# Kernel tuning notes

Hardware: AMD Instinct MI355X
Metric: run time of the kernel (lower is better)

## Reference

```python
import jax, jax.numpy as jnp
import numpy as np
from jax import lax

B, S = 64, 512
CHAR_N, CTYPE_N, BICHAR_N = 20000, 8, 200000
EXTCHAR_N, EXTBICHAR_N = 20000, 200000
D_CHAR, D_EXTCHAR, D_BICHAR, D_EXTBICHAR, D_CTYPE = 200, 200, 200, 200, 50
IN_DIM = D_CHAR + D_EXTCHAR + D_BICHAR + D_EXTBICHAR + D_CTYPE  # 850
HID, RNN_H = 512, 512


def setup_inputs() -> dict:
    key = jax.random.key(0)
    ks = jax.random.split(key, 24)
    idx = lambda k, n: jax.random.randint(k, (B, S), 0, n, dtype=jnp.int32)
    w = lambda k, shape: (jax.random.normal(k, shape, dtype=jnp.float32) * 0.02)
    return {
        'char_idx': idx(ks[0], CHAR_N),
        'char_type_idx': idx(ks[1], CTYPE_N),
        'leftbichar_idx': idx(ks[2], BICHAR_N),
        'rightbichar_idx': idx(ks[3], BICHAR_N),
        'extchar_idx': idx(ks[4], EXTCHAR_N),
        'leftextbichar_idx': idx(ks[5], EXTBICHAR_N),
        'rightextbichar_idx': idx(ks[6], EXTBICHAR_N),
        'charEmb': w(ks[7], (CHAR_N, D_CHAR)),
        'charTypeEmb': w(ks[8], (CTYPE_N, D_CTYPE)),
        'bicharEmb': w(ks[9], (BICHAR_N, D_BICHAR)),
        'extCharEmb': w(ks[10], (EXTCHAR_N, D_EXTCHAR)),
        'extBiCharEmb': w(ks[11], (EXTBICHAR_N, D_EXTBICHAR)),
        'W_lin': w(ks[12], (HID, IN_DIM)),
        'b_lin': w(ks[13], (HID,)),
        'W_ih_l': w(ks[14], (4 * RNN_H, HID)),
        'W_hh_l': w(ks[15], (4 * RNN_H, RNN_H)),
        'b_ih_l': w(ks[16], (4 * RNN_H,)),
        'b_hh_l': w(ks[17], (4 * RNN_H,)),
        'W_ih_r': w(ks[18], (4 * RNN_H, HID)),
        'W_hh_r': w(ks[19], (4 * RNN_H, RNN_H)),
        'b_ih_r': w(ks[20], (4 * RNN_H,)),
        'b_hh_r': w(ks[21], (4 * RNN_H,)),
    }


def _lstm(xg_sb4h, W_hh, reverse):
    # xg_sb4h: [S, B, 4H] precomputed input-to-gate projections (+ both biases)
    def step(carry, g_in):
        h, c = carry
        g = g_in + h @ W_hh.T  # [B, 4H]
        i, f, gg, o = jnp.split(g, 4, axis=-1)
        c = jax.nn.sigmoid(f) * c + jax.nn.sigmoid(i) * jnp.tanh(gg)
        h = jax.nn.sigmoid(o) * jnp.tanh(c)
        return (h, c), h
    h0 = jnp.zeros((xg_sb4h.shape[1], W_hh.shape[1]), xg_sb4h.dtype)
    _, hs = lax.scan(step, (h0, h0), xg_sb4h, reverse=reverse)
    return hs  # [S, B, H], hs[t] = hidden emitted at position t


def _encoder_fwd(char_idx, char_type_idx, leftbichar_idx, rightbichar_idx,
                 extchar_idx, leftextbichar_idx, rightextbichar_idx,
                 charEmb, charTypeEmb, bicharEmb, extCharEmb, extBiCharEmb,
                 W_lin, b_lin, W_ih_l, W_hh_l, b_ih_l, b_hh_l,
                 W_ih_r, W_hh_r, b_ih_r, b_hh_r):
    char = charEmb[char_idx]            # [B,S,200]
    ctype = charTypeEmb[char_type_idx]  # [B,S,50]
    extChar = extCharEmb[extchar_idx]
    leftBi = bicharEmb[leftbichar_idx]
    rightBi = bicharEmb[rightbichar_idx]
    leftExtBi = extBiCharEmb[leftextbichar_idx]
    rightExtBi = extBiCharEmb[rightextbichar_idx]
    # dropout is identity in eval mode
    leftCat = jnp.concatenate([char, extChar, leftBi, leftExtBi, ctype], axis=-1)
    rightCat = jnp.concatenate([char, extChar, rightBi, rightExtBi, ctype], axis=-1)
    leftIn = jnp.tanh(leftCat @ W_lin.T + b_lin)    # [B,S,HID]
    rightIn = jnp.tanh(rightCat @ W_lin.T + b_lin)  # [B,S,HID]
    xg_l = (jnp.einsum('bsh,gh->sbg', leftIn, W_ih_l) + b_ih_l + b_hh_l)
    xg_r = (jnp.einsum('bsh,gh->sbg', rightIn, W_ih_r) + b_ih_r + b_hh_r)
    hs_l = _lstm(xg_l, W_hh_l, reverse=False).swapaxes(0, 1)  # [B,S,RNN_H]
    hs_r = _lstm(xg_r, W_hh_r, reverse=True).swapaxes(0, 1)   # [B,S,RNN_H]
    return jnp.concatenate([hs_l, hs_r], axis=-1)  # [B,S,2*RNN_H]


def reference(char_idx, char_type_idx, leftbichar_idx, rightbichar_idx,
              extchar_idx, leftextbichar_idx, rightextbichar_idx,
              charEmb, charTypeEmb, bicharEmb, extCharEmb, extBiCharEmb,
              W_lin, b_lin, W_ih_l, W_hh_l, b_ih_l, b_hh_l,
              W_ih_r, W_hh_r, b_ih_r, b_hh_r):
    return _encoder_fwd(char_idx, char_type_idx, leftbichar_idx, rightbichar_idx,
                        extchar_idx, leftextbichar_idx, rightextbichar_idx,
                        charEmb, charTypeEmb, bicharEmb, extCharEmb, extBiCharEmb,
                        W_lin, b_lin, W_ih_l, W_hh_l, b_ih_l, b_hh_l,
                        W_ih_r, W_hh_r, b_ih_r, b_hh_r)
```

## Files before the change

### kernel.cpp

```cpp
#include <hip/hip_runtime.h>

#define INPUTS_BF16 0
#define OUT_BF16    0

typedef unsigned int  u32;
typedef unsigned short u16;
typedef unsigned long long u64;
typedef short bf16x8 __attribute__((ext_vector_type(8)));
typedef float f32x4  __attribute__((ext_vector_type(4)));
typedef unsigned int u32x4 __attribute__((ext_vector_type(4)));

__device__ __forceinline__ float bf2f(u16 x) {
  return __uint_as_float(((u32)x) << 16);
}
__device__ __forceinline__ u16 f2bf(float f) {
  u32 u = __float_as_uint(f);
  u += 0x7fffu + ((u >> 16) & 1u);
  return (u16)(u >> 16);
}

__device__ __forceinline__ u32 tload2(const void* tab, long idx2) {
#if INPUTS_BF16
  return ((const u32*)tab)[idx2];
#else
  float2 v = ((const float2*)tab)[idx2];
  return (u32)f2bf(v.x) | ((u32)f2bf(v.y) << 16);
#endif
}
__device__ __forceinline__ u16 wload(const void* w, long idx) {
#if INPUTS_BF16
  return ((const u16*)w)[idx];
#else
  return f2bf(((const float*)w)[idx]);
#endif
}
__device__ __forceinline__ float wloadf(const void* w, long idx) {
#if INPUTS_BF16
  return bf2f(((const u16*)w)[idx]);
#else
  return ((const float*)w)[idx];
#endif
}

__device__ __forceinline__ u32 aload32(const u32* p) {
  return __hip_atomic_load(p, __ATOMIC_RELAXED, __HIP_MEMORY_SCOPE_AGENT);
}
__device__ __forceinline__ u64 aload64(const u64* p) {
  return __hip_atomic_load(p, __ATOMIC_RELAXED, __HIP_MEMORY_SCOPE_AGENT);
}
__device__ __forceinline__ void astore32(u32* p, u32 v) {
  __hip_atomic_store(p, v, __ATOMIC_RELAXED, __HIP_MEMORY_SCOPE_AGENT);
}

__device__ __forceinline__ void async16(const u16* g, const u16* lds) {
  __builtin_amdgcn_global_load_lds((const __attribute__((address_space(1))) void*)g,
                                   (__attribute__((address_space(3))) void*)lds, 16, 0, 0);
}

#define Bb   64
#define Ss   512
#define BS   32768
#define KPAD 896
#define HID  512
#define G4   2048

#define OFF_CAT   0ull
#define OFF_WLIN  117440512ull
#define OFF_WIH   118358016ull
#define OFF_WHH   122552320ull
#define OFF_B4    126746624ull
#define OFF_IN    126763008ull
#define OFF_XG    193871872ull
#define OFF_HBUF  462307328ull
#define OFF_CNT   462831616ull
#define WS_NEED   462835712ull

__global__ __launch_bounds__(256) void k_prep(
    const void* Wlin_in,
    const void* Wihl, const void* Whhl, const void* bihl, const void* bhhl,
    const void* Wihr, const void* Whhr, const void* bihr, const void* bhhr,
    u16* __restrict__ Wlin, u16* __restrict__ Wih, u16* __restrict__ Whh,
    float* __restrict__ b4, u16* __restrict__ hbuf, u32* __restrict__ cnt) {
  int i = blockIdx.x * 256 + threadIdx.x;
  const int N1 = 512 * KPAD;
  const int N2 = N1 + 2 * G4 * HID;
  const int N3 = N2 + 2 * G4 * HID;
  const int N4 = N3 + 2 * G4;
  const int N5 = N4 + 2 * 2 * Bb * HID;
  const int N6 = N5 + 1024;
  if (i < N1) {
    int n = i / KPAD, k = i - n * KPAD;
    Wlin[i] = (k < 850) ? wload(Wlin_in, (long)n * 850 + k) : (u16)0;
  } else if (i < N2) {
    int j = i - N1;
    int dir = j >> 20;
    int rem = j & ((1 << 20) - 1);
    int np_ = rem >> 9, k = rem & 511;
    int orig = (np_ & 3) * 512 + (np_ >> 2);
    Wih[j] = wload(dir ? Wihr : Wihl, (long)orig * 512 + k);
  } else if (i < N3) {
    int j = i - N2;
    int dir = j >> 20;
    int rem = j & ((1 << 20) - 1);
    int np_ = rem >> 9, k = rem & 511;
    int orig = (np_ & 3) * 512 + (np_ >> 2);
    Whh[j] = wload(dir ? Whhr : Whhl, (long)orig * 512 + k);
  } else if (i < N4) {
    int j = i - N3;
    int dir = j >> 11, np_ = j & 2047;
    int orig = (np_ & 3) * 512 + (np_ >> 2);
    b4[j] = wloadf(dir ? bihr : bihl, orig) + wloadf(dir ? bhhr : bhhl, orig);
  } else if (i < N5) {
    hbuf[i - N4] = 0;
  } else if (i < N6) {
    cnt[i - N5] = 0;
  }
}

__global__ __launch_bounds__(256) void k_gather(
    const int* __restrict__ ci, const int* __restrict__ cti,
    const int* __restrict__ lbi, const int* __restrict__ rbi,
    const int* __restrict__ eci, const int* __restrict__ lebi, const int* __restrict__ rebi,
    const void* __restrict__ charE, const void* __restrict__ ctypeE,
    const void* __restrict__ biE, const void* __restrict__ extE, const void* __restrict__ extbiE,
    u32* __restrict__ cat) {
  int p = blockIdx.x;
  int t = threadIdx.x;
  u32* L = cat + (size_t)p * 448;
  u32* R = cat + (size_t)(BS + p) * 448;
  long c0 = (long)ci[p] * 100,  e0 = (long)eci[p] * 100;
  long lb0 = (long)lbi[p] * 100, rb0 = (long)rbi[p] * 100;
  long le0 = (long)lebi[p] * 100, re0 = (long)rebi[p] * 100;
  long ct0 = (long)cti[p] * 25;
  for (int c = t; c < 448; c += 256) {
    u32 vl, vr;
    if (c < 100)      { vl = vr = tload2(charE,  c0 + c); }
    else if (c < 200) { vl = vr = tload2(extE,   e0 + c - 100); }
    else if (c < 300) { vl = tload2(biE,  lb0 + c - 200); vr = tload2(biE,  rb0 + c - 200); }
    else if (c < 400) { vl = tload2(extbiE, le0 + c - 300); vr = tload2(extbiE, re0 + c - 300); }
    else if (c < 425) { vl = vr = tload2(ctypeE, ct0 + c - 400); }
    else              { vl = vr = 0u; }
    L[c] = vl; R[c] = vr;
  }
}

__global__ __launch_bounds__(256) void k_gemm1(
    const u16* __restrict__ cat, const u16* __restrict__ wlin,
    const void* __restrict__ blin, u16* __restrict__ IN) {
  __shared__ __align__(16) u16 As[128 * 64];
  __shared__ __align__(16) u16 Bs[128 * 64];
  const int tid = threadIdx.x, w = tid >> 6, l = tid & 63;
  const int m0 = blockIdx.x * 128, n0 = blockIdx.y * 128;
  const int wm = w >> 1, wn = w & 1;
  f32x4 acc[4][4] = {};
  for (int k0 = 0; k0 < KPAD; k0 += 64) {
    #pragma unroll
    for (int it = 0; it < 4; ++it) {
      int rw = it * 32 + w * 8;
      int row = rw + (l >> 3);
      int q = (l & 7) ^ (row & 7);
      async16(cat  + (size_t)(m0 + row) * KPAD + k0 + q * 8, &As[rw * 64]);
      async16(wlin + (size_t)(n0 + row) * KPAD + k0 + q * 8, &Bs[rw * 64]);
    }
    __builtin_amdgcn_s_waitcnt(0);
    __syncthreads();
    #pragma unroll
    for (int kk = 0; kk < 2; ++kk) {
      bf16x8 av[4], bv[4];
      #pragma unroll
      for (int mt = 0; mt < 4; ++mt) {
        int row = wm * 64 + mt * 16 + (l & 15);
        int cg = kk * 4 + (l >> 4);
        av[mt] = *(const bf16x8*)&As[row * 64 + ((cg ^ (row & 7)) << 3)];
      }
      #pragma unroll
      for (int nt = 0; nt < 4; ++nt) {
        int row = wn * 64 + nt * 16 + (l & 15);
        int cg = kk * 4 + (l >> 4);
        bv[nt] = *(const bf16x8*)&Bs[row * 64 + ((cg ^ (row & 7)) << 3)];
      }
      #pragma unroll
      for (int mt = 0; mt < 4; ++mt)
        #pragma unroll
        for (int nt = 0; nt < 4; ++nt)
          acc[mt][nt] = __builtin_amdgcn_mfma_f32_16x16x32_bf16(av[mt], bv[nt], acc[mt][nt], 0, 0, 0);
    }
    __syncthreads();
  }
  #pragma unroll
  for (int nt = 0; nt < 4; ++nt) {
    int col = n0 + wn * 64 + nt * 16 + (l & 15);
    float bb = wloadf(blin, col);
    #pragma unroll
    for (int mt = 0; mt < 4; ++mt)
      #pragma unroll
      for (int r = 0; r < 4; ++r) {
        int row = m0 + wm * 64 + mt * 16 + (l >> 4) * 4 + r;
        IN[(size_t)row * 512 + col] = f2bf(tanhf(acc[mt][nt][r] + bb));
      }
  }
}

__global__ __launch_bounds__(256) void k_gemm2(
    const u16* __restrict__ IN, const u16* __restrict__ wih,
    const float* __restrict__ b4, u16* __restrict__ xg) {
  __shared__ __align__(16) u16 As[128 * 64];
  __shared__ __align__(16) u16 Bs[128 * 64];
  const int tid = threadIdx.x, w = tid >> 6, l = tid & 63;
  const int m0 = blockIdx.x * 128, n0 = blockIdx.y * 128, dir = blockIdx.z;
  const int wm = w >> 1, wn = w & 1;
  f32x4 acc[4][4] = {};
  for (int k0 = 0; k0 < 512; k0 += 64) {
    #pragma unroll
    for (int it = 0; it < 4; ++it) {
      int rw = it * 32 + w * 8;
      int row = rw + (l >> 3);
      int q = (l & 7) ^ (row & 7);
      async16(IN  + (size_t)(dir * BS + m0 + row) * 512 + k0 + q * 8, &As[rw * 64]);
      async16(wih + (size_t)(dir * G4 + n0 + row) * 512 + k0 + q * 8, &Bs[rw * 64]);
    }
    __builtin_amdgcn_s_waitcnt(0);
    __syncthreads();
    #pragma unroll
    for (int kk = 0; kk < 2; ++kk) {
      bf16x8 av[4], bv[4];
      #pragma unroll
      for (int mt = 0; mt < 4; ++mt) {
        int row = wm * 64 + mt * 16 + (l & 15);
        int cg = kk * 4 + (l >> 4);
        av[mt] = *(const bf16x8*)&As[row * 64 + ((cg ^ (row & 7)) << 3)];
      }
      #pragma unroll
      for (int nt = 0; nt < 4; ++nt) {
        int row = wn * 64 + nt * 16 + (l & 15);
        int cg = kk * 4 + (l >> 4);
        bv[nt] = *(const bf16x8*)&Bs[row * 64 + ((cg ^ (row & 7)) << 3)];
      }
      #pragma unroll
      for (int mt = 0; mt < 4; ++mt)
        #pragma unroll
        for (int nt = 0; nt < 4; ++nt)
          acc[mt][nt] = __builtin_amdgcn_mfma_f32_16x16x32_bf16(av[mt], bv[nt], acc[mt][nt], 0, 0, 0);
    }
    __syncthreads();
  }
  #pragma unroll
  for (int nt = 0; nt < 4; ++nt) {
    int col = n0 + wn * 64 + nt * 16 + (l & 15);
    float bb = b4[dir * G4 + col];
    #pragma unroll
    for (int mt = 0; mt < 4; ++mt)
      #pragma unroll
      for (int r = 0; r < 4; ++r) {
        int pos = m0 + wm * 64 + mt * 16 + (l >> 4) * 4 + r;
        int s = pos & 511, b = pos >> 9;
        xg[(((size_t)dir * 512 + s) * 64 + b) * G4 + col] = f2bf(acc[mt][nt][r] + bb);
      }
  }
}

__global__ __launch_bounds__(256) void k_rnn(
    const u16* __restrict__ xg, const u16* __restrict__ whh,
    u16* __restrict__ hbuf, u32* __restrict__ cnt, float* __restrict__ out) {
  __shared__ __align__(16) u16 Hs[32 * 520];
  __shared__ float garr[32 * 66];
  __shared__ float cs[32 * 16];
  const int tid = threadIdx.x, w = tid >> 6, l = tid & 63;
  const int bid = blockIdx.x;
  const int dir = bid >> 6;
  const int sub = bid & 63;
  const int chunk = sub >> 1;
  const int half = sub & 1;
  const int b0 = half * 32;

  bf16x8 wf[16];
  const u16* wbase = whh + ((size_t)dir * G4 + chunk * 64 + w * 16 + (l & 15)) * 512;
  #pragma unroll
  for (int ks = 0; ks < 16; ++ks)
    wf[ks] = *(const bf16x8*)(wbase + ks * 32 + (l >> 4) * 8);

  for (int i = tid; i < 32 * 16; i += 256) cs[i] = 0.f;
  __syncthreads();

  u32* slots = cnt + (size_t)(dir * 2 + half) * 32;

  u16 xr[2][4];
  {
    const int t0 = dir ? 511 : 0;
    const u16* a0 = xg + (((size_t)dir * 512 + t0) * 64 + b0) * G4 + chunk * 64 + w * 16 + (l & 15);
    #pragma unroll
    for (int mt = 0; mt < 2; ++mt)
      #pragma unroll
      for (int r = 0; r < 4; ++r)
        xr[mt][r] = a0[(size_t)(mt * 16 + (l >> 4) * 4 + r) * G4];
  }

  for (int p = 0; p < 512; ++p) {
    if (p > 0) {
      if (tid < 32) {
        while (aload32(&slots[tid]) < (u32)p) { }
      }
      __syncthreads();
      asm volatile("" ::: "memory");
    }
    const int t_eff = dir ? (511 - p) : p;
    const int par = p & 1;

    const u16* hsrc = hbuf + ((size_t)(dir * 2 + par) * Bb + b0) * 512;
    #pragma unroll
    for (int it = 0; it < 8; ++it) {
      int row = w * 8 + it;
      const u64* src = (const u64*)(hsrc + (size_t)row * 512);
      u64 v0 = aload64(src + l * 2);
      u64 v1 = aload64(src + l * 2 + 1);
      u32x4 vv;
      vv.x = (u32)v0; vv.y = (u32)(v0 >> 32);
      vv.z = (u32)v1; vv.w = (u32)(v1 >> 32);
      *(u32x4*)&Hs[row * 520 + l * 8] = vv;
    }
    __syncthreads();

    f32x4 acc2[2] = {};
    #pragma unroll
    for (int ks = 0; ks < 16; ++ks) {
      #pragma unroll
      for (int mt = 0; mt < 2; ++mt) {
        int row = mt * 16 + (l & 15);
        bf16x8 a = *(const bf16x8*)&Hs[row * 520 + ks * 32 + (l >> 4) * 8];
        acc2[mt] = __builtin_amdgcn_mfma_f32_16x16x32_bf16(a, wf[ks], acc2[mt], 0, 0, 0);
      }
    }

    #pragma unroll
    for (int mt = 0; mt < 2; ++mt)
      #pragma unroll
      for (int r = 0; r < 4; ++r) {
        float g = acc2[mt][r] + bf2f(xr[mt][r]);
        int tp = l & 3;
        float v = (tp == 2) ? tanhf(g) : 1.f / (1.f + __expf(-g));
        garr[(mt * 16 + (l >> 4) * 4 + r) * 66 + w * 16 + (l & 15)] = v;
      }
    __syncthreads();

    float h0, h1;
    int b = tid >> 3, jp = tid & 7;
    {
      const float* gp = &garr[b * 66 + jp * 8];
      float i0 = gp[0], f0 = gp[1], g0 = gp[2], o0 = gp[3];
      float i1 = gp[4], f1 = gp[5], g1 = gp[6], o1 = gp[7];
      float c0v = f0 * cs[b * 16 + jp * 2]     + i0 * g0;
      float c1v = f1 * cs[b * 16 + jp * 2 + 1] + i1 * g1;
      cs[b * 16 + jp * 2] = c0v;
      cs[b * 16 + jp * 2 + 1] = c1v;
      h0 = o0 * tanhf(c0v); h1 = o1 * tanhf(c1v);
      u32 packed = (u32)f2bf(h0) | ((u32)f2bf(h1) << 16);
      astore32(&((u32*)hbuf)[(((size_t)(dir * 2 + (1 - par)) * Bb + b0 + b) * 512 + chunk * 16 + jp * 2) >> 1],
               packed);
    }

    asm volatile("s_waitcnt vmcnt(0)" ::: "memory");
    __syncthreads();
    if (tid == 0) astore32(&slots[chunk], (u32)(p + 1));

    {
#if OUT_BF16
      u32 packed = (u32)f2bf(h0) | ((u32)f2bf(h1) << 16);
      ((u32*)out)[(((size_t)(b0 + b) * 512 + t_eff) * 1024 + dir * 512 + chunk * 16 + jp * 2) >> 1] = packed;
#else
      size_t oi = ((size_t)(b0 + b) * 512 + t_eff) * 1024 + dir * 512 + chunk * 16 + jp * 2;
      float2 o2; o2.x = h0; o2.y = h1;
      *(float2*)&out[oi] = o2;
#endif
    }

    {
      int pn = (p < 511) ? (p + 1) : 511;
      int tn = dir ? (511 - pn) : pn;
      const u16* a2 = xg + (((size_t)dir * 512 + tn) * 64 + b0) * G4 + chunk * 64 + w * 16 + (l & 15);
      #pragma unroll
      for (int mt = 0; mt < 2; ++mt)
        #pragma unroll
        for (int r = 0; r < 4; ++r)
          xr[mt][r] = a2[(size_t)(mt * 16 + (l >> 4) * 4 + r) * G4];
    }
  }
}

extern "C" void kernel_launch(void* const* d_in, const int* in_sizes, int n_in,
                              void* d_out, int out_size, void* d_ws, size_t ws_size,
                              hipStream_t stream) {
  if (ws_size < WS_NEED) return;
  char* ws = (char*)d_ws;
  u16*   cat_h = (u16*)(ws + OFF_CAT);
  u16*   wlin  = (u16*)(ws + OFF_WLIN);
  u16*   wih   = (u16*)(ws + OFF_WIH);
  u16*   whh   = (u16*)(ws + OFF_WHH);
  float* b4    = (float*)(ws + OFF_B4);
  u16*   IN    = (u16*)(ws + OFF_IN);
  u16*   xgb   = (u16*)(ws + OFF_XG);
  u16*   hbuf  = (u16*)(ws + OFF_HBUF);
  u32*   cnt   = (u32*)(ws + OFF_CNT);

  k_prep<<<18708, 256, 0, stream>>>(
      d_in[12], d_in[14], d_in[15], d_in[16], d_in[17],
      d_in[18], d_in[19], d_in[20], d_in[21],
      wlin, wih, whh, b4, hbuf, cnt);

  k_gather<<<BS, 256, 0, stream>>>(
      (const int*)d_in[0], (const int*)d_in[1], (const int*)d_in[2], (const int*)d_in[3],
      (const int*)d_in[4], (const int*)d_in[5], (const int*)d_in[6],
      d_in[7], d_in[8], d_in[9], d_in[10], d_in[11], (u32*)cat_h);

  k_gemm1<<<dim3(512, 4), 256, 0, stream>>>(cat_h, wlin, d_in[13], IN);

  k_gemm2<<<dim3(256, 16, 2), 256, 0, stream>>>(IN, wih, b4, xgb);

  k_rnn<<<128, 256, 0, stream>>>(xgb, whh, hbuf, cnt, (float*)d_out);
}
```

Before: 3.666 ms.

## Halve RNN block count with wider per-block gate chunks and padded sync slots

The recurrent kernel now runs 64 blocks instead of 128. Each block computes 128 gate columns (two MFMA N-tiles per wave), so fewer blocks take part in the per-step cross-block barrier. Sync counters are padded to separate cache lines, and tanhf is replaced by an exp-based fast tanh. Stores of h and the output are widened to 64-bit and 128-bit. The cost is twice the MFMA work per block per step, more registers, and an explicit wait on the xg prefetch each step.

```diff
diff --git a/kernel.cpp b/kernel.cpp
--- a/kernel.cpp
+++ b/kernel.cpp
@@ -18,6 +18,9 @@
   u += 0x7fffu + ((u >> 16) & 1u);
   return (u16)(u >> 16);
 }
+
+__device__ __forceinline__ float sigm(float x) { return 1.f / (1.f + __expf(-x)); }
+__device__ __forceinline__ float tanh_fast(float x) { return 2.f / (1.f + __expf(-2.f * x)) - 1.f; }
 
 __device__ __forceinline__ u32 tload2(const void* tab, long idx2) {
 #if INPUTS_BF16
@@ -49,6 +52,9 @@
   return __hip_atomic_load(p, __ATOMIC_RELAXED, __HIP_MEMORY_SCOPE_AGENT);
 }
 __device__ __forceinline__ void astore32(u32* p, u32 v) {
+  __hip_atomic_store(p, v, __ATOMIC_RELAXED, __HIP_MEMORY_SCOPE_AGENT);
+}
+__device__ __forceinline__ void astore64(u64* p, u64 v) {
   __hip_atomic_store(p, v, __ATOMIC_RELAXED, __HIP_MEMORY_SCOPE_AGENT);
 }
 
@@ -259,46 +265,52 @@
   }
 }
 
-__global__ __launch_bounds__(256) void k_rnn(
+__global__ __launch_bounds__(256, 1) void k_rnn(
     const u16* __restrict__ xg, const u16* __restrict__ whh,
     u16* __restrict__ hbuf, u32* __restrict__ cnt, float* __restrict__ out) {
   __shared__ __align__(16) u16 Hs[32 * 520];
-  __shared__ float garr[32 * 66];
-  __shared__ float cs[32 * 16];
+  __shared__ __align__(16) float garr[32 * 132];
+  __shared__ __align__(16) float cs[32 * 32];
   const int tid = threadIdx.x, w = tid >> 6, l = tid & 63;
   const int bid = blockIdx.x;
-  const int dir = bid >> 6;
-  const int sub = bid & 63;
+  const int dir = bid >> 5;
+  const int sub = bid & 31;
   const int chunk = sub >> 1;
   const int half = sub & 1;
   const int b0 = half * 32;
 
-  bf16x8 wf[16];
-  const u16* wbase = whh + ((size_t)dir * G4 + chunk * 64 + w * 16 + (l & 15)) * 512;
+  bf16x8 wf[2][16];
   #pragma unroll
-  for (int ks = 0; ks < 16; ++ks)
-    wf[ks] = *(const bf16x8*)(wbase + ks * 32 + (l >> 4) * 8);
-
-  for (int i = tid; i < 32 * 16; i += 256) cs[i] = 0.f;
+  for (int nt = 0; nt < 2; ++nt) {
+    const u16* wb = whh + ((size_t)dir * G4 + chunk * 128 + w * 32 + nt * 16 + (l & 15)) * 512;
+    #pragma unroll
+    for (int ks = 0; ks < 16; ++ks)
+      wf[nt][ks] = *(const bf16x8*)(wb + ks * 32 + (l >> 4) * 8);
+  }
+
+  for (int i = tid; i < 32 * 32; i += 256) cs[i] = 0.f;
   __syncthreads();
 
-  u32* slots = cnt + (size_t)(dir * 2 + half) * 32;
-
-  u16 xr[2][4];
+  u32* slots = cnt + (size_t)(dir * 2 + half) * 256;
+
+  u16 xr[2][2][4];
   {
     const int t0 = dir ? 511 : 0;
-    const u16* a0 = xg + (((size_t)dir * 512 + t0) * 64 + b0) * G4 + chunk * 64 + w * 16 + (l & 15);
+    const u16* a0 = xg + (((size_t)dir * 512 + t0) * 64 + b0) * G4 + chunk * 128 + w * 32 + (l & 15);
     #pragma unroll
     for (int mt = 0; mt < 2; ++mt)
       #pragma unroll
-      for (int r = 0; r < 4; ++r)
-        xr[mt][r] = a0[(size_t)(mt * 16 + (l >> 4) * 4 + r) * G4];
-  }
+      for (int nt = 0; nt < 2; ++nt)
+        #pragma unroll
+        for (int r = 0; r < 4; ++r)
+          xr[mt][nt][r] = a0[(size_t)(mt * 16 + (l >> 4) * 4 + r) * G4 + nt * 16];
+  }
+  asm volatile("s_waitcnt vmcnt(0)" ::: "memory");
 
   for (int p = 0; p < 512; ++p) {
     if (p > 0) {
-      if (tid < 32) {
-        while (aload32(&slots[tid]) < (u32)p) { }
+      if (tid < 16) {
+        while (aload32(&slots[tid * 16]) < (u32)p) { }
       }
       __syncthreads();
       asm volatile("" ::: "memory");
@@ -320,69 +332,71 @@
     }
     __syncthreads();
 
-    f32x4 acc2[2] = {};
+    f32x4 acc2[2][2] = {};
     #pragma unroll
     for (int ks = 0; ks < 16; ++ks) {
       #pragma unroll
       for (int mt = 0; mt < 2; ++mt) {
-        int row = mt * 16 + (l & 15);
-        bf16x8 a = *(const bf16x8*)&Hs[row * 520 + ks * 32 + (l >> 4) * 8];
-        acc2[mt] = __builtin_amdgcn_mfma_f32_16x16x32_bf16(a, wf[ks], acc2[mt], 0, 0, 0);
+        bf16x8 a = *(const bf16x8*)&Hs[(mt * 16 + (l & 15)) * 520 + ks * 32 + (l >> 4) * 8];
+        acc2[mt][0] = __builtin_amdgcn_mfma_f32_16x16x32_bf16(a, wf[0][ks], acc2[mt][0], 0, 0, 0);
+        acc2[mt][1] = __builtin_amdgcn_mfma_f32_16x16x32_bf16(a, wf[1][ks], acc2[mt][1], 0, 0, 0);
       }
     }
 
     #pragma unroll
     for (int mt = 0; mt < 2; ++mt)
       #pragma unroll
-      for (int r = 0; r < 4; ++r) {
-        float g = acc2[mt][r] + bf2f(xr[mt][r]);
-        int tp = l & 3;
-        float v = (tp == 2) ? tanhf(g) : 1.f / (1.f + __expf(-g));
-        garr[(mt * 16 + (l >> 4) * 4 + r) * 66 + w * 16 + (l & 15)] = v;
-      }
-    __syncthreads();
-
-    float h0, h1;
-    int b = tid >> 3, jp = tid & 7;
+      for (int nt = 0; nt < 2; ++nt)
+        #pragma unroll
+        for (int r = 0; r < 4; ++r) {
+          float g = acc2[mt][nt][r] + bf2f(xr[mt][nt][r]);
+          float v = ((l & 3) == 2) ? tanh_fast(g) : sigm(g);
+          garr[(mt * 16 + (l >> 4) * 4 + r) * 132 + w * 32 + nt * 16 + (l & 15)] = v;
+        }
+    __syncthreads();
+
+    const int b = tid >> 3, jp = tid & 7;
+    float h[4];
     {
-      const float* gp = &garr[b * 66 + jp * 8];
-      float i0 = gp[0], f0 = gp[1], g0 = gp[2], o0 = gp[3];
-      float i1 = gp[4], f1 = gp[5], g1 = gp[6], o1 = gp[7];
-      float c0v = f0 * cs[b * 16 + jp * 2]     + i0 * g0;
-      float c1v = f1 * cs[b * 16 + jp * 2 + 1] + i1 * g1;
-      cs[b * 16 + jp * 2] = c0v;
-      cs[b * 16 + jp * 2 + 1] = c1v;
-      h0 = o0 * tanhf(c0v); h1 = o1 * tanhf(c1v);
-      u32 packed = (u32)f2bf(h0) | ((u32)f2bf(h1) << 16);
-      astore32(&((u32*)hbuf)[(((size_t)(dir * 2 + (1 - par)) * Bb + b0 + b) * 512 + chunk * 16 + jp * 2) >> 1],
+      const f32x4* g4 = (const f32x4*)&garr[b * 132 + jp * 16];
+      f32x4 cc = *(const f32x4*)&cs[b * 32 + jp * 4];
+      f32x4 cn;
+      #pragma unroll
+      for (int k = 0; k < 4; ++k) {
+        f32x4 gv = g4[k];
+        float cv = gv.y * cc[k] + gv.x * gv.z;
+        cn[k] = cv;
+        h[k] = gv.w * tanh_fast(cv);
+      }
+      *(f32x4*)&cs[b * 32 + jp * 4] = cn;
+      u64 packed = (u64)f2bf(h[0]) | ((u64)f2bf(h[1]) << 16)
+                 | ((u64)f2bf(h[2]) << 32) | ((u64)f2bf(h[3]) << 48);
+      astore64((u64*)&hbuf[((size_t)(dir * 2 + (1 - par)) * Bb + b0 + b) * 512 + chunk * 32 + jp * 4],
                packed);
     }
 
     asm volatile("s_waitcnt vmcnt(0)" ::: "memory");
     __syncthreads();
-    if (tid == 0) astore32(&slots[chunk], (u32)(p + 1));
+    if (tid == 0) astore32(&slots[chunk * 16], (u32)(p + 1));
 
     {
-#if OUT_BF16
-      u32 packed = (u32)f2bf(h0) | ((u32)f2bf(h1) << 16);
-      ((u32*)out)[(((size_t)(b0 + b) * 512 + t_eff) * 1024 + dir * 512 + chunk * 16 + jp * 2) >> 1] = packed;
-#else
-      size_t oi = ((size_t)(b0 + b) * 512 + t_eff) * 1024 + dir * 512 + chunk * 16 + jp * 2;
-      float2 o2; o2.x = h0; o2.y = h1;
-      *(float2*)&out[oi] = o2;
-#endif
+      float4 o4; o4.x = h[0]; o4.y = h[1]; o4.z = h[2]; o4.w = h[3];
+      *(float4*)&out[((size_t)(b0 + b) * 512 + t_eff) * 1024 + dir * 512 + chunk * 32 + jp * 4] = o4;
     }
 
     {
       int pn = (p < 511) ? (p + 1) : 511;
       int tn = dir ? (511 - pn) : pn;
-      const u16* a2 = xg + (((size_t)dir * 512 + tn) * 64 + b0) * G4 + chunk * 64 + w * 16 + (l & 15);
+      const u16* a2 = xg + (((size_t)dir * 512 + tn) * 64 + b0) * G4 + chunk * 128 + w * 32 + (l & 15);
       #pragma unroll
       for (int mt = 0; mt < 2; ++mt)
         #pragma unroll
-        for (int r = 0; r < 4; ++r)
-          xr[mt][r] = a2[(size_t)(mt * 16 + (l >> 4) * 4 + r) * G4];
-    }
+        for (int nt = 0; nt < 2; ++nt)
+          #pragma unroll
+          for (int r = 0; r < 4; ++r)
+            xr[mt][nt][r] = a2[(size_t)(mt * 16 + (l >> 4) * 4 + r) * G4 + nt * 16];
+    }
+    asm volatile("s_waitcnt vmcnt(0)" ::: "memory");
   }
 }
 
@@ -415,5 +429,5 @@
 
   k_gemm2<<<dim3(256, 16, 2), 256, 0, stream>>>(IN, wih, b4, xgb);
 
-  k_rnn<<<128, 256, 0, stream>>>(xgb, whh, hbuf, cnt, (float*)d_out);
-}
+  k_rnn<<<64, 256, 0, stream>>>(xgb, whh, hbuf, cnt, (float*)d_out);
+}
```

Result: slower. 4.055 ms (+10.6%).
